# Kernel optimization log

Measured on AMD Instinct MI355X. Metric: run time of the kernel, lower is better.

The kernel has to match this reference:

```python
import jax, jax.numpy as jnp
import numpy as np

NUM_HEADS = 16
THETA = 10000.0


def _rope(x, pos, theta):
    # x: [B, H, S, D], pos: [S] ints. Interleaved-pair RoPE.
    D = x.shape[-1]
    half = D // 2
    inv_freq = theta ** (-(jnp.arange(half, dtype=jnp.float32) * 2.0) / D)  # [half]
    ang = pos.astype(jnp.float32)[:, None] * inv_freq[None, :]              # [S, half]
    cos, sin = jnp.cos(ang), jnp.sin(ang)
    x1 = x[..., 0::2]
    x2 = x[..., 1::2]
    r1 = x1 * cos - x2 * sin
    r2 = x1 * sin + x2 * cos
    return jnp.stack([r1, r2], axis=-1).reshape(x.shape)


def setup_inputs() -> dict:
    key = jax.random.key(0)
    ks = jax.random.split(key, 5)
    B, S, D = 4, 2048, 1024
    scale = 1.0 / np.sqrt(D)
    x = jax.random.normal(ks[0], (B, S, D), dtype=jnp.float32)
    Wq = jax.random.normal(ks[1], (D, D), dtype=jnp.float32) * scale
    Wk = jax.random.normal(ks[2], (D, D), dtype=jnp.float32) * scale
    Wv = jax.random.normal(ks[3], (D, D), dtype=jnp.float32) * scale
    Wo = jax.random.normal(ks[4], (D, D), dtype=jnp.float32) * scale
    token_positions = jnp.arange(S, dtype=jnp.int64)
    return {"x": x, "Wq": Wq, "Wk": Wk, "Wv": Wv, "Wo": Wo,
            "token_positions": token_positions}


def reference(x, Wq, Wk, Wv, Wo, token_positions):
    B, S, D = x.shape
    H = NUM_HEADS
    hd = D // H
    # Projections (weights stored as [d_model, d_k], matching the transposed params)
    q = jnp.einsum('bsd,de->bse', x, Wq).reshape(B, S, H, hd).transpose(0, 2, 1, 3)
    k = jnp.einsum('bsd,de->bse', x, Wk).reshape(B, S, H, hd).transpose(0, 2, 1, 3)
    v = jnp.einsum('bsd,de->bse', x, Wv).reshape(B, S, H, hd).transpose(0, 2, 1, 3)
    # RoPE on q and k
    q = _rope(q, token_positions, THETA)
    k = _rope(k, token_positions, THETA)
    # Causal scaled dot-product attention
    scores = jnp.einsum('bhqd,bhkd->bhqk', q, k) / jnp.sqrt(jnp.float32(hd))
    causal = jnp.tril(jnp.ones((S, S), dtype=bool))
    scores = jnp.where(causal, scores, jnp.float32(-jnp.inf))
    attn = jax.nn.softmax(scores, axis=-1)
    o = jnp.einsum('bhqk,bhkd->bhqd', attn, v)          # [B, H, S, hd]
    o = o.transpose(0, 2, 1, 3).reshape(B, S, D)         # [B, S, D]
    return jnp.einsum('bsd,de->bse', o, Wo)
```

## Files before the change

kernel.cpp:

```cpp
#include <hip/hip_runtime.h>
#include <math.h>

#define B_ 4
#define S_ 2048
#define D_ 1024
#define H_ 16
#define HD_ 64
#define ES_F 0.180336880111f
#define KF (-0.41524101186f)

typedef unsigned short ushort_t;
typedef __attribute__((ext_vector_type(8))) short short8;
typedef __attribute__((ext_vector_type(4))) short short4_t;
typedef __attribute__((ext_vector_type(4))) float f32x4;
typedef __attribute__((ext_vector_type(16))) float f32x16;

typedef const void __attribute__((address_space(1))) gvoid;
typedef void __attribute__((address_space(3))) lvoid;

__device__ __forceinline__ ushort_t f2bf(float f) {
    union { float f; unsigned u; } v; v.f = f;
    unsigned r = (v.u + 0x7FFFu + ((v.u >> 16) & 1u)) >> 16;
    return (ushort_t)r;
}
__device__ __forceinline__ float fexp2(float x) {
#if __has_builtin(__builtin_amdgcn_exp2f)
    return __builtin_amdgcn_exp2f(x);
#else
    return exp2f(x);
#endif
}
__device__ __forceinline__ unsigned pk2t(float a, float b) {
    union { float f; unsigned u; } A, Bv; A.f = a; Bv.f = b;
#if __has_builtin(__builtin_amdgcn_perm)
    return __builtin_amdgcn_perm(Bv.u, A.u, 0x07060302u);
#else
    return (A.u >> 16) | (Bv.u & 0xFFFF0000u);
#endif
}
__device__ __forceinline__ short8 mk_frag(unsigned a, unsigned b, unsigned c, unsigned d) {
    union { unsigned u[4]; short8 s; } t;
    t.u[0] = a; t.u[1] = b; t.u[2] = c; t.u[3] = d; return t.s;
}

__global__ __launch_bounds__(256)
void cvt_x(const float* __restrict__ x, ushort_t* __restrict__ xb)
{
    const size_t i = ((size_t)blockIdx.x * 256 + threadIdx.x) * 8;
    float4 a = *(const float4*)&x[i];
    float4 b = *(const float4*)&x[i + 4];
    short8 o;
    o[0] = (short)f2bf(a.x); o[1] = (short)f2bf(a.y);
    o[2] = (short)f2bf(a.z); o[3] = (short)f2bf(a.w);
    o[4] = (short)f2bf(b.x); o[5] = (short)f2bf(b.y);
    o[6] = (short)f2bf(b.z); o[7] = (short)f2bf(b.w);
    *(short8*)&xb[i] = o;
}

__global__ __launch_bounds__(256)
void cvt_wt4(const float* __restrict__ W0, const float* __restrict__ W1,
             const float* __restrict__ W2, const float* __restrict__ W3,
             ushort_t* __restrict__ T0, ushort_t* __restrict__ T1,
             ushort_t* __restrict__ T2, ushort_t* __restrict__ T3)
{
    const int z = blockIdx.z;
    const float* W = (z == 0) ? W0 : (z == 1) ? W1 : (z == 2) ? W2 : W3;
    ushort_t* Wt = (z == 0) ? T0 : (z == 1) ? T1 : (z == 2) ? T2 : T3;

    __shared__ __align__(16) float T[64 * 68];
    const int t = threadIdx.x;
    const int k0 = blockIdx.y * 64, n0 = blockIdx.x * 64;
    const int row = t >> 2, c0 = (t & 3) * 16;
#pragma unroll
    for (int u = 0; u < 4; ++u)
        *(float4*)&T[row * 68 + c0 + u * 4] =
            *(const float4*)&W[(size_t)(k0 + row) * D_ + n0 + c0 + u * 4];
    __syncthreads();
    const int n = t >> 2, kc = (t & 3) * 16;
    short8 o0, o1;
#pragma unroll
    for (int kk = 0; kk < 8; ++kk) o0[kk] = (short)f2bf(T[(kc + kk) * 68 + n]);
#pragma unroll
    for (int kk = 0; kk < 8; ++kk) o1[kk] = (short)f2bf(T[(kc + 8 + kk) * 68 + n]);
    *(short8*)&Wt[(size_t)(n0 + n) * D_ + k0 + kc] = o0;
    *(short8*)&Wt[(size_t)(n0 + n) * D_ + k0 + kc + 8] = o1;
}

__global__ __launch_bounds__(256)
void gemm_bt(const ushort_t* __restrict__ A,
             const ushort_t* __restrict__ W0, const ushort_t* __restrict__ W1,
             const ushort_t* __restrict__ W2,
             void* __restrict__ d0, void* __restrict__ d1, void* __restrict__ d2,
             const int mode_base)
{
    __shared__ __align__(16) ushort_t As[128 * 64];
    __shared__ __align__(16) ushort_t Bs[128 * 64];

    const int tid = threadIdx.x;
    const int lane = tid & 63;
    const int w = tid >> 6, wr = w >> 1, wc = w & 1;
    const int z = blockIdx.z;
    const ushort_t* Wt = (z == 0) ? W0 : (z == 1) ? W1 : W2;
    const int mode = mode_base + z;
    const int m0 = blockIdx.x * 128, n0 = blockIdx.y * 128;

    f32x4 acc[4][4];
    const f32x4 zv = {0.f, 0.f, 0.f, 0.f};
#pragma unroll
    for (int i = 0; i < 4; i++)
#pragma unroll
        for (int j = 0; j < 4; j++) acc[i][j] = zv;

    const int srow = lane >> 3;
    const int spc  = lane & 7;
    const int sch  = (spc ^ (srow & 7)) * 8;

    for (int k0 = 0; k0 < D_; k0 += 64) {
        __syncthreads();
#pragma unroll
        for (int i = 0; i < 4; ++i) {
            const int rb = (i * 4 + w) * 8;
            const ushort_t* ga = &A[(size_t)(m0 + rb + srow) * D_ + k0 + sch];
            __builtin_amdgcn_global_load_lds((gvoid*)ga, (lvoid*)&As[rb * 64], 16, 0, 0);
            const ushort_t* gb = &Wt[(size_t)(n0 + rb + srow) * D_ + k0 + sch];
            __builtin_amdgcn_global_load_lds((gvoid*)gb, (lvoid*)&Bs[rb * 64], 16, 0, 0);
        }
        __syncthreads();

#pragma unroll
        for (int kk2 = 0; kk2 < 2; ++kk2) {
            const int ch = kk2 * 4 + (lane >> 4);
            const int xr = (ch ^ (lane & 7)) << 3;
            short8 af[4], bfr[4];
#pragma unroll
            for (int rt = 0; rt < 4; ++rt)
                af[rt] = *(const short8*)&As[(wr * 64 + rt * 16 + (lane & 15)) * 64 + xr];
#pragma unroll
            for (int ct = 0; ct < 4; ++ct)
                bfr[ct] = *(const short8*)&Bs[(wc * 64 + ct * 16 + (lane & 15)) * 64 + xr];
#pragma unroll
            for (int rt = 0; rt < 4; ++rt)
#pragma unroll
                for (int ct = 0; ct < 4; ++ct)
                    acc[rt][ct] = __builtin_amdgcn_mfma_f32_16x16x32_bf16(
                        af[rt], bfr[ct], acc[rt][ct], 0, 0, 0);
        }
    }

#pragma unroll
    for (int rt = 0; rt < 4; ++rt) {
        const int mb = m0 + wr * 64 + rt * 16 + (lane >> 4) * 4;
#pragma unroll
        for (int ct = 0; ct < 4; ++ct) {
            const int n = n0 + wc * 64 + ct * 16 + (lane & 15);
            if (mode == 3) {
#pragma unroll
                for (int r = 0; r < 4; ++r)
                    ((float*)d0)[(size_t)(mb + r) * D_ + n] = acc[rt][ct][r];
            } else if (mode == 2) {
                const int bb = mb >> 11, s0 = mb & (S_ - 1);
                const int h = n >> 6, d = n & 63;
                short4_t pk;
#pragma unroll
                for (int r = 0; r < 4; ++r) pk[r] = (short)f2bf(acc[rt][ct][r]);
                *(short4_t*)&((ushort_t*)d2)[(((size_t)bb * H_ + h) * HD_ + d) * S_ + s0] = pk;
            } else {
                const int h = n >> 6, dd = n & 63;
                const int j = dd >> 1;
                const float invf = exp2f(KF * (float)j);
                ushort_t* dst = (mode == 0) ? (ushort_t*)d0 : (ushort_t*)d1;
                const float sc = (mode == 0) ? ES_F : 1.0f;
#pragma unroll
                for (int r = 0; r < 4; ++r) {
                    const int m = mb + r;
                    const int bb = m >> 11, s = m & (S_ - 1);
                    const float val = acc[rt][ct][r];
                    float sn, cs;
                    __sincosf((float)s * invf, &sn, &cs);
                    const float par = __shfl_xor(val, 1);
                    const float res = ((dd & 1) == 0) ? (val * cs - par * sn)
                                                      : (par * sn + val * cs);
                    dst[(((size_t)bb * H_ + h) * S_ + s) * HD_ + dd] = f2bf(res * sc);
                }
            }
        }
    }
}

__global__ __launch_bounds__(256)
void attn_mfma(const ushort_t* __restrict__ Q, const ushort_t* __restrict__ K,
               const ushort_t* __restrict__ Vt, ushort_t* __restrict__ O)
{
    __shared__ __align__(16) ushort_t sK[64 * 64];
    __shared__ __align__(16) ushort_t sVt[64 * 64];

    const int tid = threadIdx.x;
    const int lane = tid & 63;
    const int hl = lane >> 5;
    const int lq = lane & 31;
    const int w = tid >> 6;
    const int hb64 = blockIdx.x;
    const int pair = blockIdx.y;
    const int h = hb64 >> 2, bb = hb64 & 3;
    const size_t hb = ((size_t)(bb * H_ + h)) * S_ * HD_;

    const int srow = lane >> 3;
    const int spc = lane & 7;

    short8 ones;
#pragma unroll
    for (int i = 0; i < 8; ++i) ones[i] = (short)0x3F80;

    const f32x16 zv16 = {0,0,0,0,0,0,0,0,0,0,0,0,0,0,0,0};

    for (int pass = 0; pass < 2; ++pass) {
        const int q0 = ((pass == 0) ? (15 - pair) : pair) * 128;
        const int wq = q0 + w * 32;
        const int qg = wq + lq;

        short8 qf[4];
#pragma unroll
        for (int ks = 0; ks < 4; ++ks)
            qf[ks] = *(const short8*)&Q[hb + (size_t)qg * HD_ + ks * 16 + hl * 8];

        f32x16 oa[2], la;
        oa[0] = zv16; oa[1] = zv16; la = zv16;

        const int nt = q0 / 64 + 2;
        for (int kt = 0; kt < nt; ++kt) {
            const int k0 = kt * 64;
            __syncthreads();
            {
#pragma unroll
                for (int i = 0; i < 2; ++i) {
                    const int row = i * 32 + w * 8 + srow;
                    const int sc = (spc ^ (row & 7)) * 8;
                    __builtin_amdgcn_global_load_lds(
                        (gvoid*)&K[hb + (size_t)(k0 + row) * HD_ + sc],
                        (lvoid*)&sK[(i * 32 + w * 8) * 64], 16, 0, 0);
                    __builtin_amdgcn_global_load_lds(
                        (gvoid*)&Vt[hb + (size_t)row * S_ + k0 + sc],
                        (lvoid*)&sVt[(i * 32 + w * 8) * 64], 16, 0, 0);
                }
            }
            __syncthreads();

            if (k0 > wq + 31) continue;

            f32x16 st[2];
            st[0] = zv16; st[1] = zv16;
            const int kr0 = lq, kr1 = 32 + lq;
#pragma unroll
            for (int ks = 0; ks < 4; ++ks) {
                const int ch = ks * 2 + hl;
                short8 ak0 = *(const short8*)&sK[kr0 * 64 + ((ch ^ (kr0 & 7)) << 3)];
                short8 ak1 = *(const short8*)&sK[kr1 * 64 + ((ch ^ (kr1 & 7)) << 3)];
                st[0] = __builtin_amdgcn_mfma_f32_32x32x16_bf16(ak0, qf[ks], st[0], 0, 0, 0);
                st[1] = __builtin_amdgcn_mfma_f32_32x32x16_bf16(ak1, qf[ks], st[1], 0, 0, 0);
            }

            const bool diag = (k0 + 63 > wq);
            short8 pf[4];
#pragma unroll
            for (int nt2 = 0; nt2 < 2; ++nt2) {
                float pv[16];
                const int kb = k0 + nt2 * 32 + 4 * hl;
#pragma unroll
                for (int g = 0; g < 4; ++g)
#pragma unroll
                    for (int r = 0; r < 4; ++r) {
                        float s = st[nt2][4 * g + r];
                        if (diag) {
                            const int key = kb + 8 * g + r;
                            s = (key <= qg) ? s : -INFINITY;
                        }
                        pv[4 * g + r] = fexp2(s);
                    }
                unsigned P2[8], X[8];
#pragma unroll
                for (int g = 0; g < 4; ++g) {
                    P2[2 * g]     = pk2t(pv[4 * g + 0], pv[4 * g + 1]);
                    P2[2 * g + 1] = pk2t(pv[4 * g + 2], pv[4 * g + 3]);
                }
#pragma unroll
                for (int m = 0; m < 8; ++m) X[m] = (unsigned)__shfl_xor((int)P2[m], 32);
                pf[nt2 * 2 + 0] = hl ? mk_frag(X[2], X[3], P2[2], P2[3])
                                     : mk_frag(P2[0], P2[1], X[0], X[1]);
                pf[nt2 * 2 + 1] = hl ? mk_frag(X[6], X[7], P2[6], P2[7])
                                     : mk_frag(P2[4], P2[5], X[4], X[5]);
            }

            const int vr0 = lq, vr1 = 32 + lq;
#pragma unroll
            for (int ks2 = 0; ks2 < 4; ++ks2) {
                const int ch = ks2 * 2 + hl;
                short8 av0 = *(const short8*)&sVt[vr0 * 64 + ((ch ^ (vr0 & 7)) << 3)];
                short8 av1 = *(const short8*)&sVt[vr1 * 64 + ((ch ^ (vr1 & 7)) << 3)];
                oa[0] = __builtin_amdgcn_mfma_f32_32x32x16_bf16(av0, pf[ks2], oa[0], 0, 0, 0);
                oa[1] = __builtin_amdgcn_mfma_f32_32x32x16_bf16(av1, pf[ks2], oa[1], 0, 0, 0);
                la    = __builtin_amdgcn_mfma_f32_32x32x16_bf16(ones, pf[ks2], la, 0, 0, 0);
            }
        }

        const float inv = 1.f / la[0];
        ushort_t* Ob = &O[((size_t)(bb * S_ + qg)) * D_ + h * HD_];
#pragma unroll
        for (int mt = 0; mt < 2; ++mt)
#pragma unroll
            for (int g = 0; g < 4; ++g) {
                short4_t pk;
#pragma unroll
                for (int r = 0; r < 4; ++r)
                    pk[r] = (short)f2bf(oa[mt][4 * g + r] * inv);
                *(short4_t*)&Ob[mt * 32 + 8 * g + 4 * hl] = pk;
            }
    }
}

extern "C" void kernel_launch(void* const* d_in, const int* in_sizes, int n_in,
                              void* d_out, int out_size, void* d_ws, size_t ws_size,
                              hipStream_t stream)
{
    (void)in_sizes; (void)n_in; (void)out_size; (void)ws_size;
    const float* x  = (const float*)d_in[0];
    const float* Wq = (const float*)d_in[1];
    const float* Wk = (const float*)d_in[2];
    const float* Wv = (const float*)d_in[3];
    const float* Wo = (const float*)d_in[4];

    float* out = (float*)d_out;
    ushort_t* ws = (ushort_t*)d_ws;
    const size_t NX = (size_t)B_ * S_ * D_;
    const size_t NW = (size_t)D_ * D_;
    ushort_t* xb  = ws;
    ushort_t* Wqt = xb + NX;
    ushort_t* Wkt = Wqt + NW;
    ushort_t* Wvt = Wkt + NW;
    ushort_t* Wot = Wvt + NW;
    ushort_t* Qb  = Wot + NW;
    ushort_t* Kb  = Qb + NX;
    ushort_t* Vtb = Kb + NX;
    ushort_t* Ob  = Vtb + NX;

    cvt_x<<<dim3(NX / 2048), 256, 0, stream>>>(x, xb);
    cvt_wt4<<<dim3(16, 16, 4), 256, 0, stream>>>(Wq, Wk, Wv, Wo, Wqt, Wkt, Wvt, Wot);

    gemm_bt<<<dim3(64, 8, 3), 256, 0, stream>>>(xb, Wqt, Wkt, Wvt, Qb, Kb, Vtb, 0);
    attn_mfma<<<dim3(64, 8), 256, 0, stream>>>(Qb, Kb, Vtb, Ob);
    gemm_bt<<<dim3(64, 8, 1), 256, 0, stream>>>(Ob, Wot, Wot, Wot, out, nullptr, nullptr, 3);
}
```

Measured before the change: 262.4 us.

## Use 32x32 MFMA in projection GEMM, angle recurrence for RoPE, permlane32 swap

Switches the projection GEMM from 16x16x32 to 32x32x16 bf16 MFMA tiles, which cuts the number of LDS fragment loads per k-step, and remaps the epilogues to the new accumulator layout. The RoPE epilogue now computes one sincos per group of four rows and advances the angle with a rotation recurrence, trading transcendental calls for a little accumulated rounding error. In attention, the P-fragment exchange uses the permlane32_swap builtin when it is available, replacing eight ds_bpermute shuffles and the lane-dependent selects.

```diff
diff --git a/kernel.cpp b/kernel.cpp
--- a/kernel.cpp
+++ b/kernel.cpp
@@ -14,6 +14,7 @@
 typedef __attribute__((ext_vector_type(4))) short short4_t;
 typedef __attribute__((ext_vector_type(4))) float f32x4;
 typedef __attribute__((ext_vector_type(16))) float f32x16;
+typedef __attribute__((ext_vector_type(2))) unsigned uint2v;
 
 typedef const void __attribute__((address_space(1))) gvoid;
 typedef void __attribute__((address_space(3))) lvoid;
@@ -98,18 +99,17 @@
 
     const int tid = threadIdx.x;
     const int lane = tid & 63;
+    const int hl = lane >> 5;
+    const int lq = lane & 31;
     const int w = tid >> 6, wr = w >> 1, wc = w & 1;
     const int z = blockIdx.z;
     const ushort_t* Wt = (z == 0) ? W0 : (z == 1) ? W1 : W2;
     const int mode = mode_base + z;
     const int m0 = blockIdx.x * 128, n0 = blockIdx.y * 128;
 
-    f32x4 acc[4][4];
-    const f32x4 zv = {0.f, 0.f, 0.f, 0.f};
-#pragma unroll
-    for (int i = 0; i < 4; i++)
-#pragma unroll
-        for (int j = 0; j < 4; j++) acc[i][j] = zv;
+    const f32x16 zv16 = {0,0,0,0,0,0,0,0,0,0,0,0,0,0,0,0};
+    f32x16 acc[2][2];
+    acc[0][0] = zv16; acc[0][1] = zv16; acc[1][0] = zv16; acc[1][1] = zv16;
 
     const int srow = lane >> 3;
     const int spc  = lane & 7;
@@ -128,59 +128,73 @@
         __syncthreads();
 
 #pragma unroll
-        for (int kk2 = 0; kk2 < 2; ++kk2) {
-            const int ch = kk2 * 4 + (lane >> 4);
-            const int xr = (ch ^ (lane & 7)) << 3;
-            short8 af[4], bfr[4];
-#pragma unroll
-            for (int rt = 0; rt < 4; ++rt)
-                af[rt] = *(const short8*)&As[(wr * 64 + rt * 16 + (lane & 15)) * 64 + xr];
-#pragma unroll
-            for (int ct = 0; ct < 4; ++ct)
-                bfr[ct] = *(const short8*)&Bs[(wc * 64 + ct * 16 + (lane & 15)) * 64 + xr];
-#pragma unroll
-            for (int rt = 0; rt < 4; ++rt)
-#pragma unroll
-                for (int ct = 0; ct < 4; ++ct)
-                    acc[rt][ct] = __builtin_amdgcn_mfma_f32_16x16x32_bf16(
-                        af[rt], bfr[ct], acc[rt][ct], 0, 0, 0);
+        for (int ks = 0; ks < 4; ++ks) {
+            const int ch = ks * 2 + hl;
+            const int xr = (ch ^ (lq & 7)) << 3;
+            short8 af[2], bfr[2];
+#pragma unroll
+            for (int t = 0; t < 2; ++t) {
+                af[t]  = *(const short8*)&As[(wr * 64 + t * 32 + lq) * 64 + xr];
+                bfr[t] = *(const short8*)&Bs[(wc * 64 + t * 32 + lq) * 64 + xr];
+            }
+#pragma unroll
+            for (int tm = 0; tm < 2; ++tm)
+#pragma unroll
+                for (int tn = 0; tn < 2; ++tn)
+                    acc[tm][tn] = __builtin_amdgcn_mfma_f32_32x32x16_bf16(
+                        af[tm], bfr[tn], acc[tm][tn], 0, 0, 0);
         }
     }
 
 #pragma unroll
-    for (int rt = 0; rt < 4; ++rt) {
-        const int mb = m0 + wr * 64 + rt * 16 + (lane >> 4) * 4;
-#pragma unroll
-        for (int ct = 0; ct < 4; ++ct) {
-            const int n = n0 + wc * 64 + ct * 16 + (lane & 15);
+    for (int tn = 0; tn < 2; ++tn) {
+        const int n = n0 + wc * 64 + tn * 32 + lq;
+        const int h = n >> 6, dd = n & 63;
+        const int j = dd >> 1;
+        const float invf = exp2f(KF * (float)j);
+        float sd, cd;
+        __sincosf(invf, &sd, &cd);
+#pragma unroll
+        for (int tm = 0; tm < 2; ++tm) {
+            const int mb = m0 + wr * 64 + tm * 32 + 4 * hl;
             if (mode == 3) {
 #pragma unroll
-                for (int r = 0; r < 4; ++r)
-                    ((float*)d0)[(size_t)(mb + r) * D_ + n] = acc[rt][ct][r];
+                for (int g = 0; g < 4; ++g)
+#pragma unroll
+                    for (int r = 0; r < 4; ++r)
+                        ((float*)d0)[(size_t)(mb + 8 * g + r) * D_ + n] =
+                            acc[tm][tn][4 * g + r];
             } else if (mode == 2) {
-                const int bb = mb >> 11, s0 = mb & (S_ - 1);
-                const int h = n >> 6, d = n & 63;
-                short4_t pk;
-#pragma unroll
-                for (int r = 0; r < 4; ++r) pk[r] = (short)f2bf(acc[rt][ct][r]);
-                *(short4_t*)&((ushort_t*)d2)[(((size_t)bb * H_ + h) * HD_ + d) * S_ + s0] = pk;
+#pragma unroll
+                for (int g = 0; g < 4; ++g) {
+                    const int m_base = mb + 8 * g;
+                    const int bb = m_base >> 11, s0 = m_base & (S_ - 1);
+                    short4_t pk;
+#pragma unroll
+                    for (int r = 0; r < 4; ++r) pk[r] = (short)f2bf(acc[tm][tn][4 * g + r]);
+                    *(short4_t*)&((ushort_t*)d2)[(((size_t)bb * H_ + h) * HD_ + dd) * S_ + s0] = pk;
+                }
             } else {
-                const int h = n >> 6, dd = n & 63;
-                const int j = dd >> 1;
-                const float invf = exp2f(KF * (float)j);
                 ushort_t* dst = (mode == 0) ? (ushort_t*)d0 : (ushort_t*)d1;
                 const float sc = (mode == 0) ? ES_F : 1.0f;
 #pragma unroll
-                for (int r = 0; r < 4; ++r) {
-                    const int m = mb + r;
-                    const int bb = m >> 11, s = m & (S_ - 1);
-                    const float val = acc[rt][ct][r];
+                for (int g = 0; g < 4; ++g) {
+                    const int m_base = mb + 8 * g;
+                    const int bb = m_base >> 11, s0 = m_base & (S_ - 1);
                     float sn, cs;
-                    __sincosf((float)s * invf, &sn, &cs);
-                    const float par = __shfl_xor(val, 1);
-                    const float res = ((dd & 1) == 0) ? (val * cs - par * sn)
-                                                      : (par * sn + val * cs);
-                    dst[(((size_t)bb * H_ + h) * S_ + s) * HD_ + dd] = f2bf(res * sc);
+                    __sincosf((float)s0 * invf, &sn, &cs);
+                    ushort_t* dp = &dst[(((size_t)bb * H_ + h) * S_ + s0) * HD_ + dd];
+#pragma unroll
+                    for (int r = 0; r < 4; ++r) {
+                        const float val = acc[tm][tn][4 * g + r];
+                        const float par = __shfl_xor(val, 1);
+                        const float res = ((dd & 1) == 0) ? (val * cs - par * sn)
+                                                          : (par * sn + val * cs);
+                        dp[(size_t)r * HD_] = f2bf(res * sc);
+                        const float c2 = cs * cd - sn * sd;
+                        sn = sn * cd + cs * sd;
+                        cs = c2;
+                    }
                 }
             }
         }
@@ -276,18 +290,28 @@
                         }
                         pv[4 * g + r] = fexp2(s);
                     }
-                unsigned P2[8], X[8];
+                unsigned P2[8];
 #pragma unroll
                 for (int g = 0; g < 4; ++g) {
                     P2[2 * g]     = pk2t(pv[4 * g + 0], pv[4 * g + 1]);
                     P2[2 * g + 1] = pk2t(pv[4 * g + 2], pv[4 * g + 3]);
                 }
+#if __has_builtin(__builtin_amdgcn_permlane32_swap)
+                uint2v r02 = __builtin_amdgcn_permlane32_swap(P2[0], P2[2], false, false);
+                uint2v r13 = __builtin_amdgcn_permlane32_swap(P2[1], P2[3], false, false);
+                uint2v r46 = __builtin_amdgcn_permlane32_swap(P2[4], P2[6], false, false);
+                uint2v r57 = __builtin_amdgcn_permlane32_swap(P2[5], P2[7], false, false);
+                pf[nt2 * 2 + 0] = mk_frag(r02[0], r13[0], r02[1], r13[1]);
+                pf[nt2 * 2 + 1] = mk_frag(r46[0], r57[0], r46[1], r57[1]);
+#else
+                unsigned X[8];
 #pragma unroll
                 for (int m = 0; m < 8; ++m) X[m] = (unsigned)__shfl_xor((int)P2[m], 32);
                 pf[nt2 * 2 + 0] = hl ? mk_frag(X[2], X[3], P2[2], P2[3])
                                      : mk_frag(P2[0], P2[1], X[0], X[1]);
                 pf[nt2 * 2 + 1] = hl ? mk_frag(X[6], X[7], P2[6], P2[7])
                                      : mk_frag(P2[4], P2[5], X[4], X[5]);
+#endif
             }
 
             const int vr0 = lq, vr1 = 32 + lq;
```

Measured after the change: 251.8 us. 1.04x faster.
